# Performance work log

Measured on AMD Instinct MI355X. Metric: run time of the kernel, lower is better.

## Reference

```python
import jax, jax.numpy as jnp
import numpy as np

B, N, M, D = 32, 1024, 1024, 256


def setup_inputs() -> dict:
    key = jax.random.key(0)
    k1, k2, k3, k4 = jax.random.split(key, 4)
    h1 = jax.random.normal(k1, (B, N, D), dtype=jnp.float32)
    h2 = jax.random.normal(k2, (B, M, D), dtype=jnp.float32)
    W = jax.random.normal(k3, (D,), dtype=jnp.float32) * (1.0 / np.sqrt(D))
    b = jax.random.normal(k4, (1,), dtype=jnp.float32) * (1.0 / np.sqrt(D))
    return {"h1": h1, "h2": h2, "W": W, "b": b}


def reference(h1, h2, W, b):
    # Pairwise squared L2 distance (p=2, abs(x-y)^2 == (x-y)^2), halved as in the
    # original: dist_matrix = cdist(g1, g2) / 2.0. Use the ||x||^2+||y||^2-2xy
    # expansion to avoid materializing the [B,N,M,D] difference tensor.
    sq1 = jnp.sum(h1 * h1, axis=-1)                      # [B, N]
    sq2 = jnp.sum(h2 * h2, axis=-1)                      # [B, M]
    cross = jnp.einsum('bnd,bmd->bnm', h1, h2)           # [B, N, M]
    dist = jnp.maximum(sq1[:, :, None] + sq2[:, None, :] - 2.0 * cross, 0.0) * 0.5

    # Insertion/deletion cost: |Linear(h)| per node.
    d1 = jnp.abs(jnp.einsum('bnd,d->bn', h1, W) + b)     # [B, N]
    d2 = jnp.abs(jnp.einsum('bmd,d->bm', h2, W) + b)     # [B, M]

    a = jnp.minimum(jnp.min(dist, axis=1), d2)           # min over rows -> [B, M]
    bb = jnp.minimum(jnp.min(dist, axis=2), d1)          # min over cols -> [B, N]
    d = jnp.mean(a, axis=-1) + jnp.mean(bb, axis=-1)     # [B]
    return d
```

## Files before the change

### kernel.cpp

```cpp
#include <hip/hip_runtime.h>


#define B_  32
#define N_  1024
#define D_  256
#define BN_ (B_ * N_)
#define TILE 128
#define BK   32

typedef short bf16x8 __attribute__((ext_vector_type(8)));
typedef float f32x4  __attribute__((ext_vector_type(4)));
typedef unsigned short u16;
typedef unsigned int   u32;

__device__ __forceinline__ u16 f2bf(float x) {
  u32 u = __float_as_uint(x);
  u += 0x7fffu + ((u >> 16) & 1u);
  return (u16)(u >> 16);
}

__device__ __forceinline__ void gload16(const void* g, void* l) {
  __builtin_amdgcn_global_load_lds((const __attribute__((address_space(1))) u32*)g,
                                   (__attribute__((address_space(3))) u32*)l, 16, 0, 0);
}


__global__ __launch_bounds__(256) void prep_kernel(
    const float* __restrict__ h1, const float* __restrict__ h2,
    const float* __restrict__ W, const float* __restrict__ bias,
    u16* __restrict__ bfA, u16* __restrict__ bfB, int strideSh,
    float* __restrict__ fl) {
  const int tid = threadIdx.x, lane = tid & 63, wid = tid >> 6;
  const int bid = blockIdx.x;
  const int xcd = bid & 7;
  const int i   = bid >> 3;
  const int g   = (i >> 9) * 8 + xcd;
  const int r9  = i & 511;
  const int rows4 = r9 * 4 + wid;
  const int isB = rows4 >> 10;
  const int row = g * N_ + (rows4 & 1023);

  const float4 v = *(const float4*)((isB ? h2 : h1) + (size_t)row * D_ + lane * 4);
  const float4 w = *(const float4*)(W + lane * 4);
  float sq = v.x * v.x + v.y * v.y + v.z * v.z + v.w * v.w;
  float dw = v.x * w.x + v.y * w.y + v.z * w.z + v.w * w.w;
#pragma unroll
  for (int off = 1; off < 64; off <<= 1) {
    sq += __shfl_xor(sq, off);
    dw += __shfl_xor(dw, off);
  }

  const ushort4 o = {f2bf(v.x), f2bf(v.y), f2bf(v.z), f2bf(v.w)};
  *(ushort4*)((isB ? bfB : bfA) + (size_t)row * strideSh + lane * 4) = o;

  if (lane == 0) {
    fl[isB * BN_ + row]       = fabsf(dw + bias[0]);
    fl[(2 + isB) * BN_ + row] = sq;
  }
  if (lane == 1) ((u32*)fl)[(4 + isB) * BN_ + row] = 0x7f7f7f7fu;
}

__global__ __launch_bounds__(256) void gemm_kernel(
    const u16* __restrict__ bfA, const u16* __restrict__ bfB, int strideSh,
    float* __restrict__ fl) {
  __shared__ __align__(16) u16 As[2][TILE * BK];
  __shared__ __align__(16) u16 Bs[2][TILE * BK];
  __shared__ float sqrow[TILE], sqcol[TILE];
  __shared__ float rowred[TILE][2], colred[TILE][2];

  const int bid = blockIdx.x;
  const int b   = ((bid >> 9) << 3) + (bid & 7);
  const int t6  = (bid >> 3) & 63;
  const int bm  = t6 & 7;
  const int bn  = t6 >> 3;

  const int tid = threadIdx.x, lane = tid & 63, wid = tid >> 6;
  const int wr = wid >> 1, wc = wid & 1;

  if (tid < TILE) sqrow[tid] = fl[2 * BN_ + b * N_ + bn * TILE + tid];
  else            sqcol[tid - TILE] = fl[3 * BN_ + b * N_ + bm * TILE + (tid - TILE)];

  const char* srcA[2]; const char* srcB[2];
#pragma unroll
  for (int c = 0; c < 2; ++c) {
    const int o   = (wid * 2 + c) * 1024 + lane * 16;
    const int lin = o ^ (((o >> 6) & 7) << 4);
    const int row = lin >> 6;
    const int kb  = lin & 63;
    srcA[c] = (const char*)(bfA + (size_t)(b * N_ + bn * TILE + row) * strideSh) + kb;
    srcB[c] = (const char*)(bfB + (size_t)(b * N_ + bm * TILE + row) * strideSh) + kb;
  }

  f32x4 acc[4][4];
#pragma unroll
  for (int i = 0; i < 4; ++i)
#pragma unroll
    for (int j = 0; j < 4; ++j) acc[i][j] = (f32x4){0.f, 0.f, 0.f, 0.f};

  const int arow = wr * 64 + (lane & 15);
  const int brow = wc * 64 + (lane & 15);
  const int aoff = (arow * 64 + ((lane >> 4) * 16)) ^ ((arow & 7) << 4);
  const int boff = (brow * 64 + ((lane >> 4) * 16)) ^ ((brow & 7) << 4);

  auto stage = [&](int c) {
#pragma unroll
    for (int q = 0; q < 2; ++q) {
      gload16(srcA[q], &As[c][(wid * 2 + q) * 512]);
      gload16(srcB[q], &Bs[c][(wid * 2 + q) * 512]);
      srcA[q] += 64; srcB[q] += 64;
    }
  };
  auto compute = [&](int c) {
    const char* ab = (const char*)As[c];
    const char* bb = (const char*)Bs[c];
    bf16x8 af[4], bfv[4];
#pragma unroll
    for (int mi = 0; mi < 4; ++mi) af[mi]  = *(const bf16x8*)(ab + aoff + mi * 1024);
#pragma unroll
    for (int nj = 0; nj < 4; ++nj) bfv[nj] = *(const bf16x8*)(bb + boff + nj * 1024);
#pragma unroll
    for (int mi = 0; mi < 4; ++mi)
#pragma unroll
      for (int nj = 0; nj < 4; ++nj)
        acc[mi][nj] = __builtin_amdgcn_mfma_f32_16x16x32_bf16(af[mi], bfv[nj], acc[mi][nj], 0, 0, 0);
  };

  stage(0);
  __syncthreads();
  int cur = 0;
#pragma unroll 1
  for (int ks = 0; ks < 7; ++ks) {
    stage(cur ^ 1);
    compute(cur);
    __syncthreads();
    cur ^= 1;
  }
  compute(cur);

  float sj[4];
#pragma unroll
  for (int nj = 0; nj < 4; ++nj) sj[nj] = sqcol[wc * 64 + nj * 16 + (lane & 15)];

  float rminv[4][4];
  float cminv[4] = {3.0e38f, 3.0e38f, 3.0e38f, 3.0e38f};
#pragma unroll
  for (int mi = 0; mi < 4; ++mi)
#pragma unroll
    for (int r = 0; r < 4; ++r) {
      const float si = sqrow[wr * 64 + mi * 16 + (lane >> 4) * 4 + r];
      float rm = 3.0e38f;
#pragma unroll
      for (int nj = 0; nj < 4; ++nj) {
        const float dd = fmaxf(fmaf(-2.f, acc[mi][nj][r], si + sj[nj]), 0.f) * 0.5f;
        rm = fminf(rm, dd);
        cminv[nj] = fminf(cminv[nj], dd);
      }
      rminv[mi][r] = rm;
    }

#pragma unroll
  for (int mi = 0; mi < 4; ++mi)
#pragma unroll
    for (int r = 0; r < 4; ++r) {
      float v = rminv[mi][r];
      v = fminf(v, __shfl_xor(v, 1));
      v = fminf(v, __shfl_xor(v, 2));
      v = fminf(v, __shfl_xor(v, 4));
      v = fminf(v, __shfl_xor(v, 8));
      rminv[mi][r] = v;
    }
  if ((lane & 15) == 0) {
#pragma unroll
    for (int mi = 0; mi < 4; ++mi)
#pragma unroll
      for (int r = 0; r < 4; ++r)
        rowred[wr * 64 + mi * 16 + (lane >> 4) * 4 + r][wc] = rminv[mi][r];
  }

#pragma unroll
  for (int nj = 0; nj < 4; ++nj) {
    float v = cminv[nj];
    v = fminf(v, __shfl_xor(v, 16));
    v = fminf(v, __shfl_xor(v, 32));
    cminv[nj] = v;
  }
  if (lane < 16) {
#pragma unroll
    for (int nj = 0; nj < 4; ++nj)
      colred[wc * 64 + nj * 16 + lane][wr] = cminv[nj];
  }
  __syncthreads();

  u32* rming = (u32*)(fl + 4 * BN_);
  u32* cming = (u32*)(fl + 5 * BN_);
  if (tid < TILE) {
    const float v = fminf(rowred[tid][0], rowred[tid][1]);
    atomicMin(&rming[b * N_ + bn * TILE + tid], __float_as_uint(v));
  } else {
    const int c = tid - TILE;
    const float v = fminf(colred[c][0], colred[c][1]);
    atomicMin(&cming[b * N_ + bm * TILE + c], __float_as_uint(v));
  }
}

__global__ __launch_bounds__(256) void finish_kernel(
    const float* __restrict__ fl, float* __restrict__ out) {
  const int b = blockIdx.x;
  const int tid = threadIdx.x;
  const float* dd1  = fl + b * N_;
  const float* dd2  = fl + BN_ + b * N_;
  const float* rmin = fl + 4 * BN_ + b * N_;
  const float* cmin = fl + 5 * BN_ + b * N_;

  float s = 0.f;
  for (int i = tid; i < N_; i += 256)
    s += fminf(rmin[i], dd1[i]) + fminf(cmin[i], dd2[i]);

  __shared__ float sm[4];
  for (int off = 32; off; off >>= 1) s += __shfl_down(s, off);
  if ((tid & 63) == 0) sm[tid >> 6] = s;
  __syncthreads();
  if (tid == 0) out[b] = (sm[0] + sm[1] + sm[2] + sm[3]) * (1.f / 1024.f);
}

extern "C" void kernel_launch(void* const* d_in, const int* in_sizes, int n_in,
                              void* d_out, int out_size, void* d_ws, size_t ws_size,
                              hipStream_t stream) {
  (void)in_sizes; (void)n_in; (void)out_size;
  const float* h1   = (const float*)d_in[0];
  const float* h2   = (const float*)d_in[1];
  const float* W    = (const float*)d_in[2];
  const float* bias = (const float*)d_in[3];
  float* out = (float*)d_out;

  const size_t BF_BYTES = (size_t)BN_ * D_ * 2;
  const size_t NEED     = 2 * BF_BYTES + 6u * BN_ * 4;

  u16 *bfA, *bfB; int strideSh; float* fl;
  if (ws_size >= NEED) {
    bfA = (u16*)d_ws;
    bfB = (u16*)((char*)d_ws + BF_BYTES);
    strideSh = D_;
    fl = (float*)((char*)d_ws + 2 * BF_BYTES);
  } else {
    bfA = (u16*)d_in[0];
    bfB = (u16*)d_in[1];
    strideSh = 2 * D_;
    fl = (float*)d_ws;
  }

  prep_kernel<<<dim3(16384), 256, 0, stream>>>(h1, h2, W, bias, bfA, bfB, strideSh, fl);
  gemm_kernel<<<dim3(2048), 256, 0, stream>>>(bfA, bfB, strideSh, fl);
  finish_kernel<<<dim3(B_), 256, 0, stream>>>(fl, out);
}
```

Measured before the change: 146.3 us.

## Load MFMA fragments directly from global memory instead of LDS staging

The GEMM kernel stops staging bf16 tiles of A and B through double-buffered LDS with global_load_lds. Each wave now reads its MFMA operand fragments straight from global memory, relying on the caches for reuse, and the per-step barriers go away. This removes LDS traffic and synchronisation, but each tile row is now fetched by two waves, which raises global and L2 traffic. It also drops the explicit prefetch pipeline, leaving the compiler's unroll-by-2 to hide memory latency.

```diff
diff --git a/kernel.cpp b/kernel.cpp
--- a/kernel.cpp
+++ b/kernel.cpp
@@ -6,7 +6,6 @@
 #define D_  256
 #define BN_ (B_ * N_)
 #define TILE 128
-#define BK   32
 
 typedef short bf16x8 __attribute__((ext_vector_type(8)));
 typedef float f32x4  __attribute__((ext_vector_type(4)));
@@ -17,11 +16,6 @@
   u32 u = __float_as_uint(x);
   u += 0x7fffu + ((u >> 16) & 1u);
   return (u16)(u >> 16);
-}
-
-__device__ __forceinline__ void gload16(const void* g, void* l) {
-  __builtin_amdgcn_global_load_lds((const __attribute__((address_space(1))) u32*)g,
-                                   (__attribute__((address_space(3))) u32*)l, 16, 0, 0);
 }
 
 
@@ -63,8 +57,6 @@
 __global__ __launch_bounds__(256) void gemm_kernel(
     const u16* __restrict__ bfA, const u16* __restrict__ bfB, int strideSh,
     float* __restrict__ fl) {
-  __shared__ __align__(16) u16 As[2][TILE * BK];
-  __shared__ __align__(16) u16 Bs[2][TILE * BK];
   __shared__ float sqrow[TILE], sqcol[TILE];
   __shared__ float rowred[TILE][2], colred[TILE][2];
 
@@ -80,15 +72,14 @@
   if (tid < TILE) sqrow[tid] = fl[2 * BN_ + b * N_ + bn * TILE + tid];
   else            sqcol[tid - TILE] = fl[3 * BN_ + b * N_ + bm * TILE + (tid - TILE)];
 
-  const char* srcA[2]; const char* srcB[2];
-#pragma unroll
-  for (int c = 0; c < 2; ++c) {
-    const int o   = (wid * 2 + c) * 1024 + lane * 16;
-    const int lin = o ^ (((o >> 6) & 7) << 4);
-    const int row = lin >> 6;
-    const int kb  = lin & 63;
-    srcA[c] = (const char*)(bfA + (size_t)(b * N_ + bn * TILE + row) * strideSh) + kb;
-    srcB[c] = (const char*)(bfB + (size_t)(b * N_ + bm * TILE + row) * strideSh) + kb;
+  const char* aptr[4];
+  const char* bptr[4];
+#pragma unroll
+  for (int q = 0; q < 4; ++q) {
+    aptr[q] = (const char*)(bfA + (size_t)(b * N_ + bn * TILE + wr * 64 + q * 16 + (lane & 15)) * strideSh)
+              + ((lane >> 4) * 16);
+    bptr[q] = (const char*)(bfB + (size_t)(b * N_ + bm * TILE + wc * 64 + q * 16 + (lane & 15)) * strideSh)
+              + ((lane >> 4) * 16);
   }
 
   f32x4 acc[4][4];
@@ -97,45 +88,22 @@
 #pragma unroll
     for (int j = 0; j < 4; ++j) acc[i][j] = (f32x4){0.f, 0.f, 0.f, 0.f};
 
-  const int arow = wr * 64 + (lane & 15);
-  const int brow = wc * 64 + (lane & 15);
-  const int aoff = (arow * 64 + ((lane >> 4) * 16)) ^ ((arow & 7) << 4);
-  const int boff = (brow * 64 + ((lane >> 4) * 16)) ^ ((brow & 7) << 4);
-
-  auto stage = [&](int c) {
-#pragma unroll
-    for (int q = 0; q < 2; ++q) {
-      gload16(srcA[q], &As[c][(wid * 2 + q) * 512]);
-      gload16(srcB[q], &Bs[c][(wid * 2 + q) * 512]);
-      srcA[q] += 64; srcB[q] += 64;
-    }
-  };
-  auto compute = [&](int c) {
-    const char* ab = (const char*)As[c];
-    const char* bb = (const char*)Bs[c];
+#pragma unroll 2
+  for (int t = 0; t < 8; ++t) {
+    const int off = t * 64;
     bf16x8 af[4], bfv[4];
 #pragma unroll
-    for (int mi = 0; mi < 4; ++mi) af[mi]  = *(const bf16x8*)(ab + aoff + mi * 1024);
-#pragma unroll
-    for (int nj = 0; nj < 4; ++nj) bfv[nj] = *(const bf16x8*)(bb + boff + nj * 1024);
+    for (int mi = 0; mi < 4; ++mi) af[mi]  = *(const bf16x8*)(aptr[mi] + off);
+#pragma unroll
+    for (int nj = 0; nj < 4; ++nj) bfv[nj] = *(const bf16x8*)(bptr[nj] + off);
 #pragma unroll
     for (int mi = 0; mi < 4; ++mi)
 #pragma unroll
       for (int nj = 0; nj < 4; ++nj)
         acc[mi][nj] = __builtin_amdgcn_mfma_f32_16x16x32_bf16(af[mi], bfv[nj], acc[mi][nj], 0, 0, 0);
-  };
-
-  stage(0);
+  }
+
   __syncthreads();
-  int cur = 0;
-#pragma unroll 1
-  for (int ks = 0; ks < 7; ++ks) {
-    stage(cur ^ 1);
-    compute(cur);
-    __syncthreads();
-    cur ^= 1;
-  }
-  compute(cur);
 
   float sj[4];
 #pragma unroll
```

New measurement: 175.5 us. 1.2x slower.
